# Optimization experiments

Hardware: AMD Instinct MI355X
Metric: run time of the kernel (lower is better)

Reference implementation:

```python
import jax, jax.numpy as jnp
import numpy as np

B, N, M = 2048, 4096, 4096


def setup_inputs() -> dict:
    key = jax.random.key(0)
    kt, kv, kr = jax.random.split(key, 3)
    # sorted abscissae per sample (interp1d assumes monotone t)
    t = jnp.sort(jax.random.uniform(kt, (B, N), dtype=jnp.float32), axis=-1)
    v = jax.random.normal(kv, (B, N), dtype=jnp.float32)
    # queries slightly outside [0,1] to exercise the extrapolation clamp
    r = jax.random.uniform(kr, (B, M), minval=-0.05, maxval=1.05, dtype=jnp.float32)
    return {"t": t, "v": v, "r": r}


def _interp1(t, v, r):
    # t: [N] sorted, v: [N], r: [M]
    idx = jnp.clip(jnp.searchsorted(t, r, side='right'), 1, t.shape[0] - 1)
    t0 = t[idx - 1]
    t1 = t[idx]
    v0 = v[idx - 1]
    v1 = v[idx]
    denom = jnp.where(t1 == t0, jnp.float32(1.0), t1 - t0)
    out = v0 + (r - t0) / denom * (v1 - v0)
    # scipy fill_value=(v[0], v[-1]) with bounds_error=False: clamp extrapolation
    out = jnp.where(r < t[0], v[0], out)
    out = jnp.where(r > t[-1], v[-1], out)
    return out


def reference(t, v, r):
    # batched 1D linear interpolation with clamped extrapolation -> [B, M]
    return jax.vmap(_interp1)(t, v, r)
```

## Files before the change

kernel.cpp:

```cpp
#include <hip/hip_runtime.h>

constexpr int B = 2048;
constexpr int N = 4096;
constexpr int M = 4096;
constexpr int K = 2048;
constexpr int QPT = 16;

__global__ __launch_bounds__(256, 4) void interp_kernel(
    const float* __restrict__ t,
    const float* __restrict__ v,
    const float* __restrict__ r,
    float* __restrict__ out) {
    __shared__ float2 stv[N];
    __shared__ unsigned short lut[K + 2];

    const int b = blockIdx.x;
    const float* tb = t + (size_t)b * N;
    const float* vb = v + (size_t)b * N;
    const float* rb = r + (size_t)b * M;
    float* ob = out + (size_t)b * M;

    const float4* r4 = (const float4*)rb;
    float4 qv[QPT / 4];
    #pragma unroll
    for (int p = 0; p < QPT / 4; ++p) qv[p] = r4[threadIdx.x + 256 * p];

    for (int i = threadIdx.x; i < N / 4; i += 256) {
        const float4 t4 = ((const float4*)tb)[i];
        const float4 v4 = ((const float4*)vb)[i];
        stv[4 * i + 0] = make_float2(t4.x, v4.x);
        stv[4 * i + 1] = make_float2(t4.y, v4.y);
        stv[4 * i + 2] = make_float2(t4.z, v4.z);
        stv[4 * i + 3] = make_float2(t4.w, v4.w);
    }
    for (int k = threadIdx.x; k <= K; k += 256) lut[k] = (unsigned short)N;
    __syncthreads();

    for (int j = threadIdx.x; j < N; j += 256) {
        int khi = (int)(stv[j].x * K);
        if (khi > K - 1) khi = K - 1;
        int klo = 0;
        if (j > 0) klo = (int)(stv[j - 1].x * K) + 1;
        for (int k = klo; k <= khi; ++k) lut[k] = (unsigned short)j;
    }
    __syncthreads();

    const float tfirst = stv[0].x;
    const float vfirst = stv[0].y;
    const float tlast = stv[N - 1].x;
    const float vlast = stv[N - 1].y;

    float q[QPT];
    #pragma unroll
    for (int p = 0; p < QPT / 4; ++p) {
        q[4 * p + 0] = qv[p].x;
        q[4 * p + 1] = qv[p].y;
        q[4 * p + 2] = qv[p].z;
        q[4 * p + 3] = qv[p].w;
    }

    int lo[QPT], hi[QPT];
    #pragma unroll
    for (int j = 0; j < QPT; ++j) {
        int k = (int)(q[j] * K);
        k = k < 0 ? 0 : (k > K - 1 ? K - 1 : k);
        lo[j] = (int)lut[k];
        hi[j] = (int)lut[k + 1];
    }
    #pragma unroll
    for (int j = 0; j < QPT; ++j) {
        #pragma unroll
        for (int s = 0; s < 2; ++s) {
            const int safe = lo[j] < N - 1 ? lo[j] : N - 1;
            const bool adv = (lo[j] < hi[j]) && (stv[safe].x <= q[j]);
            lo[j] += adv ? 1 : 0;
        }
        while (lo[j] < hi[j] && stv[lo[j]].x <= q[j]) ++lo[j];
    }
    float o[QPT];
    #pragma unroll
    for (int j = 0; j < QPT; ++j) {
        const int idx = lo[j] < 1 ? 1 : (lo[j] > N - 1 ? N - 1 : lo[j]);
        const float2 p0 = stv[idx - 1];
        const float2 p1 = stv[idx];
        const float denom = (p1.x == p0.x) ? 1.0f : (p1.x - p0.x);
        float oo = p0.y + (q[j] - p0.x) / denom * (p1.y - p0.y);
        oo = (q[j] < tfirst) ? vfirst : oo;
        oo = (q[j] > tlast) ? vlast : oo;
        o[j] = oo;
    }
    float4* o4 = (float4*)ob;
    #pragma unroll
    for (int p = 0; p < QPT / 4; ++p) {
        o4[threadIdx.x + 256 * p] =
            make_float4(o[4 * p + 0], o[4 * p + 1], o[4 * p + 2], o[4 * p + 3]);
    }
}

extern "C" void kernel_launch(void* const* d_in, const int* in_sizes, int n_in,
                              void* d_out, int out_size, void* d_ws, size_t ws_size,
                              hipStream_t stream) {
    const float* t = (const float*)d_in[0];
    const float* v = (const float*)d_in[1];
    const float* r = (const float*)d_in[2];
    float* out = (float*)d_out;
    interp_kernel<<<B, 256, 0, stream>>>(t, v, r, out);
}
```

Measured before the change: 156.8 us.

## Replace LUT bounded walk with fixed six-entry window branchless select

Doubles the LUT resolution so each bucket covers about one sample. Each query then loads a fixed, aligned window of six (t,v) pairs as three float4 LDS reads and picks the bracketing pair with branchless selects. A scalar fallback loop handles the rare case where the window is exceeded. Queries are processed in four passes of four, and the shared-memory staging writes are vectorised to float4. The aim is to cut divergent dependent LDS loads and register pressure, at the cost of a larger LUT and extra wide loads per query.

```diff
diff --git a/kernel.cpp b/kernel.cpp
--- a/kernel.cpp
+++ b/kernel.cpp
@@ -3,16 +3,16 @@
 constexpr int B = 2048;
 constexpr int N = 4096;
 constexpr int M = 4096;
-constexpr int K = 2048;
-constexpr int QPT = 16;
+constexpr int K = 4096;
+constexpr int QPT = 4;
 
 __global__ __launch_bounds__(256, 4) void interp_kernel(
     const float* __restrict__ t,
     const float* __restrict__ v,
     const float* __restrict__ r,
     float* __restrict__ out) {
-    __shared__ float2 stv[N];
-    __shared__ unsigned short lut[K + 2];
+    __shared__ __align__(16) float2 stv[N];
+    __shared__ unsigned short lut[K];
 
     const int b = blockIdx.x;
     const float* tb = t + (size_t)b * N;
@@ -21,26 +21,24 @@
     float* ob = out + (size_t)b * M;
 
     const float4* r4 = (const float4*)rb;
-    float4 qv[QPT / 4];
+    float4 qv[4];
     #pragma unroll
-    for (int p = 0; p < QPT / 4; ++p) qv[p] = r4[threadIdx.x + 256 * p];
+    for (int p = 0; p < 4; ++p) qv[p] = r4[threadIdx.x + 256 * p];
 
     for (int i = threadIdx.x; i < N / 4; i += 256) {
         const float4 t4 = ((const float4*)tb)[i];
         const float4 v4 = ((const float4*)vb)[i];
-        stv[4 * i + 0] = make_float2(t4.x, v4.x);
-        stv[4 * i + 1] = make_float2(t4.y, v4.y);
-        stv[4 * i + 2] = make_float2(t4.z, v4.z);
-        stv[4 * i + 3] = make_float2(t4.w, v4.w);
+        float4* d = (float4*)&stv[4 * i];
+        d[0] = make_float4(t4.x, v4.x, t4.y, v4.y);
+        d[1] = make_float4(t4.z, v4.z, t4.w, v4.w);
     }
-    for (int k = threadIdx.x; k <= K; k += 256) lut[k] = (unsigned short)N;
+    for (int k = threadIdx.x; k < K; k += 256) lut[k] = (unsigned short)N;
     __syncthreads();
 
     for (int j = threadIdx.x; j < N; j += 256) {
         int khi = (int)(stv[j].x * K);
         if (khi > K - 1) khi = K - 1;
-        int klo = 0;
-        if (j > 0) klo = (int)(stv[j - 1].x * K) + 1;
+        const int klo = (j == 0) ? 0 : (int)(stv[j - 1].x * K) + 1;
         for (int k = klo; k <= khi; ++k) lut[k] = (unsigned short)j;
     }
     __syncthreads();
@@ -49,51 +47,59 @@
     const float vfirst = stv[0].y;
     const float tlast = stv[N - 1].x;
     const float vlast = stv[N - 1].y;
+    const float4* S4 = (const float4*)stv;
+    float4* o4 = (float4*)ob;
 
-    float q[QPT];
     #pragma unroll
-    for (int p = 0; p < QPT / 4; ++p) {
-        q[4 * p + 0] = qv[p].x;
-        q[4 * p + 1] = qv[p].y;
-        q[4 * p + 2] = qv[p].z;
-        q[4 * p + 3] = qv[p].w;
-    }
+    for (int pass = 0; pass < 4; ++pass) {
+        const float4 qp = qv[pass];
+        float q[QPT] = {qp.x, qp.y, qp.z, qp.w};
+        int w[QPT];
+        float4 W0[QPT], W1[QPT], W2[QPT];
 
-    int lo[QPT], hi[QPT];
-    #pragma unroll
-    for (int j = 0; j < QPT; ++j) {
-        int k = (int)(q[j] * K);
-        k = k < 0 ? 0 : (k > K - 1 ? K - 1 : k);
-        lo[j] = (int)lut[k];
-        hi[j] = (int)lut[k + 1];
-    }
-    #pragma unroll
-    for (int j = 0; j < QPT; ++j) {
         #pragma unroll
-        for (int s = 0; s < 2; ++s) {
-            const int safe = lo[j] < N - 1 ? lo[j] : N - 1;
-            const bool adv = (lo[j] < hi[j]) && (stv[safe].x <= q[j]);
-            lo[j] += adv ? 1 : 0;
+        for (int j = 0; j < QPT; ++j) {
+            int k = (int)(q[j] * K);
+            k = k < 0 ? 0 : (k > K - 1 ? K - 1 : k);
+            int ww = (int)lut[k] - 1;
+            ww = ww < 0 ? 0 : (ww > N - 6 ? N - 6 : ww);
+            ww &= ~1;
+            w[j] = ww;
+            const float4* p = S4 + (ww >> 1);
+            W0[j] = p[0];
+            W1[j] = p[1];
+            W2[j] = p[2];
         }
-        while (lo[j] < hi[j] && stv[lo[j]].x <= q[j]) ++lo[j];
-    }
-    float o[QPT];
-    #pragma unroll
-    for (int j = 0; j < QPT; ++j) {
-        const int idx = lo[j] < 1 ? 1 : (lo[j] > N - 1 ? N - 1 : lo[j]);
-        const float2 p0 = stv[idx - 1];
-        const float2 p1 = stv[idx];
-        const float denom = (p1.x == p0.x) ? 1.0f : (p1.x - p0.x);
-        float oo = p0.y + (q[j] - p0.x) / denom * (p1.y - p0.y);
-        oo = (q[j] < tfirst) ? vfirst : oo;
-        oo = (q[j] > tlast) ? vlast : oo;
-        o[j] = oo;
-    }
-    float4* o4 = (float4*)ob;
-    #pragma unroll
-    for (int p = 0; p < QPT / 4; ++p) {
-        o4[threadIdx.x + 256 * p] =
-            make_float4(o[4 * p + 0], o[4 * p + 1], o[4 * p + 2], o[4 * p + 3]);
+        float o[QPT];
+        #pragma unroll
+        for (int j = 0; j < QPT; ++j) {
+            const float qq = q[j];
+            const float2 P0 = make_float2(W0[j].x, W0[j].y);
+            const float2 P1 = make_float2(W0[j].z, W0[j].w);
+            const float2 P2 = make_float2(W1[j].x, W1[j].y);
+            const float2 P3 = make_float2(W1[j].z, W1[j].w);
+            const float2 P4 = make_float2(W2[j].x, W2[j].y);
+            const float2 P5 = make_float2(W2[j].z, W2[j].w);
+            const bool b1 = P1.x <= qq, b2 = P2.x <= qq, b3 = P3.x <= qq;
+            const bool b4 = P4.x <= qq, b5 = P5.x <= qq;
+            float2 plo = P0, phi = P1;
+            plo = b1 ? P1 : plo; phi = b1 ? P2 : phi;
+            plo = b2 ? P2 : plo; phi = b2 ? P3 : phi;
+            plo = b3 ? P3 : plo; phi = b3 ? P4 : phi;
+            plo = b4 ? P4 : plo; phi = b4 ? P5 : phi;
+            if (b5 && qq < tlast) {
+                int c = w[j] + 6;
+                while (c < N && stv[c].x <= qq) ++c;
+                plo = stv[c - 1];
+                phi = stv[c];
+            }
+            const float denom = (phi.x == plo.x) ? 1.0f : (phi.x - plo.x);
+            float oo = plo.y + (qq - plo.x) / denom * (phi.y - plo.y);
+            oo = (qq < tfirst) ? vfirst : oo;
+            oo = (qq >= tlast) ? vlast : oo;
+            o[j] = oo;
+        }
+        o4[threadIdx.x + 256 * pass] = make_float4(o[0], o[1], o[2], o[3]);
     }
 }
 
```

After: 152.5 us. 2.8% less time.
